# Optimization experiments

Hardware: AMD Instinct MI355X
Metric: run time of the kernel (lower is better)

Reference implementation:

```python
import jax, jax.numpy as jnp
import numpy as np

CHEB_K = 3
DIM_IN = 2
HIDDEN = 64
EMBED_DIM = 10
NODE_NUM = 2048
BATCH = 32


def _gconv(x, supports, W, b, cheb_k=CHEB_K):
    # Chebyshev graph conv applied directly to x (equivalent to building
    # T_k(A) matrices then applying: T_k(A) x = 2 A T_{k-1}(A) x - T_{k-2}(A) x).
    xs = [x, jnp.einsum('nm,bmc->bnc', supports, x)]
    for _ in range(2, cheb_k):
        xs.append(2.0 * jnp.einsum('nm,bmc->bnc', supports, xs[-1]) - xs[-2])
    x_g = jnp.concatenate(xs, axis=-1)          # [B, N, cheb_k*C]
    return jnp.einsum('bni,io->bno', x_g, W) + b


def setup_inputs() -> dict:
    key = jax.random.key(0)
    ks = jax.random.split(key, 7)
    c_in = DIM_IN + HIDDEN                       # 66
    # xavier_normal-ish scale for weights
    def xavier(k, fan_in, fan_out):
        std = float(np.sqrt(2.0 / (fan_in + fan_out)))
        return jax.random.normal(k, (fan_in, fan_out), dtype=jnp.float32) * std
    return {
        'x': jax.random.normal(ks[0], (BATCH, NODE_NUM, DIM_IN), dtype=jnp.float32),
        'state': jax.random.normal(ks[1], (BATCH, NODE_NUM, HIDDEN), dtype=jnp.float32),
        'node_embeddings': jax.random.normal(ks[2], (NODE_NUM, EMBED_DIM), dtype=jnp.float32),
        'W_gate': xavier(ks[3], CHEB_K * c_in, 2 * HIDDEN),
        'b_gate': jnp.zeros((2 * HIDDEN,), dtype=jnp.float32),
        'W_update': xavier(ks[4], CHEB_K * c_in, HIDDEN),
        'b_update': jnp.zeros((HIDDEN,), dtype=jnp.float32),
    }


def reference(x, state, node_embeddings, W_gate, b_gate, W_update, b_update):
    # adaptive adjacency: softmax(relu(E E^T), axis=1)
    logits = jnp.einsum('nc,mc->nm', node_embeddings, node_embeddings)
    supports = jax.nn.softmax(jax.nn.relu(logits), axis=1)   # [N, N]

    input_and_state = jnp.concatenate([x, state], axis=-1)   # [B, N, dim_in+hidden]
    z_r = jax.nn.sigmoid(_gconv(input_and_state, supports, W_gate, b_gate))
    z, r = jnp.split(z_r, 2, axis=-1)                        # each [B, N, hidden]
    candidate = jnp.concatenate([x, z * state], axis=-1)
    hc = jnp.tanh(_gconv(candidate, supports, W_update, b_update))
    h = r * state + (1.0 - r) * hc
    return h
```

## Files before the change

kernel.cpp:

```cpp
#include <hip/hip_runtime.h>


typedef __bf16 bf16x8 __attribute__((ext_vector_type(8)));
typedef __bf16 bf16x4 __attribute__((ext_vector_type(4)));
typedef float  f32x4  __attribute__((ext_vector_type(4)));

#define GLB(p) ((__attribute__((address_space(1))) void*)(void*)(p))
#define LDS(p) ((__attribute__((address_space(3))) void*)(p))

__global__ void prologue_kernel(const float* __restrict__ E, __bf16* __restrict__ S,
                                const float* __restrict__ Wg, __bf16* __restrict__ WTg,
                                const float* __restrict__ Wu, __bf16* __restrict__ WTu) {
    const int bid = blockIdx.x;
    const int t = threadIdx.x;
    __shared__ float sm[4], ss[4];
    if (bid >= 2048) {
        const float* W = (bid < 2176) ? Wg : Wu;
        __bf16* WT = (bid < 2176) ? WTg : WTu;
        const int Nout = (bid < 2176) ? 128 : 64;
        const int id = (bid - ((bid < 2176) ? 2048 : 2176)) * 256 + t;
        const int o = id >> 8, k = id & 255;
        const int jj = (k >= 144) ? 2 : (k >= 72 ? 1 : 0);
        const int cc = k - 72 * jj;
        const bool ok = (o < Nout) && (cc < 66) && (k < 216);
        WT[id] = ok ? (__bf16)W[(size_t)(66 * jj + cc) * Nout + o] : (__bf16)0.f;
        return;
    }
    const int n = bid;
    const int l = t & 63, w = t >> 6;
    float en[10];
#pragma unroll
    for (int i = 0; i < 10; ++i) en[i] = E[n * 10 + i];
    float vals[8];
    float mx = 0.f;
#pragma unroll
    for (int q = 0; q < 8; ++q) {
        const int m = q * 256 + t;
        const float* em = E + (size_t)m * 10;
        float d = 0.f;
#pragma unroll
        for (int i = 0; i < 10; ++i) d += en[i] * em[i];
        d = fmaxf(d, 0.f);
        vals[q] = d;
        mx = fmaxf(mx, d);
    }
#pragma unroll
    for (int off = 32; off; off >>= 1) mx = fmaxf(mx, __shfl_xor(mx, off));
    if (l == 0) sm[w] = mx;
    __syncthreads();
    mx = fmaxf(fmaxf(sm[0], sm[1]), fmaxf(sm[2], sm[3]));
    float sum = 0.f;
#pragma unroll
    for (int q = 0; q < 8; ++q) { vals[q] = __expf(vals[q] - mx); sum += vals[q]; }
#pragma unroll
    for (int off = 32; off; off >>= 1) sum += __shfl_xor(sum, off);
    if (l == 0) ss[w] = sum;
    __syncthreads();
    sum = ss[0] + ss[1] + ss[2] + ss[3];
    const float inv = 1.f / sum;
#pragma unroll
    for (int q = 0; q < 8; ++q) S[(size_t)n * 2048 + q * 256 + t] = (__bf16)(vals[q] * inv);
}

__global__ __launch_bounds__(256, 2)
void build_t2(const float* __restrict__ x, const float* __restrict__ st,
              const __bf16* __restrict__ zr, __bf16* __restrict__ T,
              __bf16* __restrict__ G) {
    __shared__ float Ls[66 * 129];
    const int b  = blockIdx.x >> 4;
    const int n0 = (blockIdx.x & 15) << 7;
    const int t = threadIdx.x;
    const size_t mb = (size_t)b * 2048 + n0;
    if (t < 128) {
        const float2 v = *(const float2*)&x[(mb + t) * 2];
        Ls[t] = v.x;
        Ls[129 + t] = v.y;
    }
#pragma unroll
    for (int r = 0; r < 8; ++r) {
        const int task = r * 256 + t;
        const int q = task & 15, n = task >> 4;
        f32x4 v = *(const f32x4*)&st[(mb + n) * 64 + q * 4];
        if (zr) {
            const bf16x4 z = *(const bf16x4*)&zr[(mb + n) * 128 + q * 4];
#pragma unroll
            for (int j = 0; j < 4; ++j) v[j] *= (float)z[j];
        }
        const int base = (2 + q * 4) * 129 + n;
#pragma unroll
        for (int j = 0; j < 4; ++j) Ls[base + j * 129] = v[j];
    }
    __syncthreads();
#pragma unroll
    for (int r = 0; r < 5; ++r) {
        const int task = r * 256 + t;
        if (task < 1056) {
            const int c = task >> 4, seg = task & 15;
            const float* src = &Ls[c * 129 + seg * 8];
            bf16x8 o;
#pragma unroll
            for (int j = 0; j < 8; ++j) o[j] = (__bf16)src[j];
            *(bf16x8*)&T[(size_t)(b * 66 + c) * 2048 + n0 + seg * 8] = o;
        }
    }
    {
        const int n = t & 127, half = t >> 7;
        const size_t grow = ((size_t)(b * 2048 + n0 + n)) * 256;
        for (int oct = half * 5; oct < (half ? 9 : 5); ++oct) {
            bf16x8 o8;
#pragma unroll
            for (int j = 0; j < 8; ++j) {
                const int cc = oct * 8 + j;
                o8[j] = (cc < 66) ? (__bf16)Ls[cc * 129 + n] : (__bf16)0.f;
            }
            *(bf16x8*)&G[grow + oct * 8] = o8;
        }
    }
}

__global__ __launch_bounds__(256, 3)
void gemm_pipe(const __bf16* __restrict__ A, int lda,
               const __bf16* __restrict__ Bt, int ldb,
               int K, int epi, int swz,
               __bf16* __restrict__ outT, const __bf16* __restrict__ subT,
               float* __restrict__ outF, const float* __restrict__ bias,
               __bf16* __restrict__ zrO, const __bf16* __restrict__ zrI,
               const float* __restrict__ state,
               __bf16* __restrict__ Gout, int gsec) {
    __shared__ __align__(16) __bf16 As[2][128 * 64];
    __shared__ __align__(16) __bf16 Bs[2][64 * 64];
    int mt, ct;
    if (swz) { mt = blockIdx.x & 15; ct = blockIdx.x >> 4; }
    else     { mt = blockIdx.x;      ct = blockIdx.y; }
    const int m0 = mt * 128, c0 = ct * 64;
    const int t = threadIdx.x;
    const int l = t & 63, w = t >> 6;
    const int wr = w >> 1, wc = w & 1;
    const int lm = l & 15, kq = l >> 4, lm7 = lm & 7;
    const int sr = l >> 3;
    const int gsw = (l & 7) ^ sr;

    f32x4 acc[4][2];
#pragma unroll
    for (int i = 0; i < 4; ++i)
#pragma unroll
        for (int j = 0; j < 2; ++j) acc[i][j] = (f32x4)0.f;

    const __bf16* Asrc = A  + (size_t)(m0 + w * 8 + sr) * lda + gsw * 8;
    const __bf16* Bsrc = Bt + (size_t)(c0 + w * 8 + sr) * ldb + gsw * 8;
    const int dstA = w * 512 + l * 8;

    auto stage = [&](int buf, int k0) {
#pragma unroll
        for (int q = 0; q < 4; ++q)
            __builtin_amdgcn_global_load_lds(GLB(Asrc + (size_t)q * 32 * lda + k0),
                                             LDS(&As[buf][q * 2048 + dstA]), 16, 0, 0);
#pragma unroll
        for (int q = 0; q < 2; ++q)
            __builtin_amdgcn_global_load_lds(GLB(Bsrc + (size_t)q * 32 * ldb + k0),
                                             LDS(&Bs[buf][q * 2048 + dstA]), 16, 0, 0);
    };
    auto compute = [&](int buf) {
        const __bf16* Ab = &As[buf][0];
        const __bf16* Bb = &Bs[buf][0];
#pragma unroll
        for (int ks = 0; ks < 2; ++ks) {
            const int ga = (((ks << 2) | kq) ^ lm7) << 3;
            bf16x8 af[4], bfr[2];
#pragma unroll
            for (int i = 0; i < 4; ++i)
                af[i] = *(const bf16x8*)&Ab[(wr * 64 + i * 16 + lm) * 64 + ga];
#pragma unroll
            for (int j = 0; j < 2; ++j)
                bfr[j] = *(const bf16x8*)&Bb[(wc * 32 + j * 16 + lm) * 64 + ga];
#pragma unroll
            for (int i = 0; i < 4; ++i)
#pragma unroll
                for (int j = 0; j < 2; ++j)
                    acc[i][j] = __builtin_amdgcn_mfma_f32_16x16x32_bf16(af[i], bfr[j], acc[i][j], 0, 0, 0);
        }
    };

    stage(0, 0);
    const int iters = K >> 6;
    for (int i = 0; i + 2 <= iters; i += 2) {
        stage(1, (i + 1) << 6);
        __builtin_amdgcn_sched_barrier(0);
        __builtin_amdgcn_s_waitcnt(0x0F76);
        __builtin_amdgcn_s_barrier();
        __builtin_amdgcn_sched_barrier(0);
        compute(0);
        __builtin_amdgcn_sched_barrier(0);
        __builtin_amdgcn_s_barrier();
        __builtin_amdgcn_sched_barrier(0);
        if (i + 2 < iters) {
            stage(0, (i + 2) << 6);
            __builtin_amdgcn_sched_barrier(0);
            __builtin_amdgcn_s_waitcnt(0x0F76);
        } else {
            __builtin_amdgcn_s_waitcnt(0x0F70);
        }
        __builtin_amdgcn_s_barrier();
        __builtin_amdgcn_sched_barrier(0);
        compute(1);
        __builtin_amdgcn_sched_barrier(0);
        if (i + 4 <= iters) {
            __builtin_amdgcn_s_barrier();
            __builtin_amdgcn_sched_barrier(0);
        }
    }

    const int rb0 = m0 + wr * 64 + kq * 4;
    const int cb0 = c0 + wc * 32 + lm;
#pragma unroll
    for (int i = 0; i < 4; ++i) {
        const int rbase = rb0 + i * 16;
#pragma unroll
        for (int j = 0; j < 2; ++j) {
            const int c = cb0 + j * 16;
            f32x4 v = acc[i][j];
            if (epi <= 1) {
                bf16x4 pk;
                if (epi == 0) {
#pragma unroll
                    for (int r = 0; r < 4; ++r) pk[r] = (__bf16)v[r];
                    *(bf16x4*)&outT[(size_t)c * 2048 + rbase] = pk;
                } else {
                    bf16x4 s = *(const bf16x4*)&subT[(size_t)c * 2048 + rbase];
#pragma unroll
                    for (int r = 0; r < 4; ++r) pk[r] = (__bf16)(2.f * v[r] - (float)s[r]);
                }
                const int b = c / 66, cc = c - b * 66;
                const size_t gb = ((size_t)(b * 2048 + rbase)) * 256 + gsec + cc;
#pragma unroll
                for (int r = 0; r < 4; ++r) Gout[gb + (size_t)r * 256] = pk[r];
            } else if (epi == 2) {
                const float bb = bias[c];
#pragma unroll
                for (int r = 0; r < 4; ++r) {
                    float xx = fminf(fmaxf(v[r] + bb, -30.f), 30.f);
                    zrO[(size_t)(rbase + r) * 128 + c] = (__bf16)(1.f / (1.f + __expf(-xx)));
                }
            } else {
                if (c < 64) {
                    const float bb = bias[c];
#pragma unroll
                    for (int r = 0; r < 4; ++r) {
                        const int m = rbase + r;
                        float xx = fminf(fmaxf(v[r] + bb, -15.f), 15.f);
                        float e = __expf(2.f * xx);
                        float hc = (e - 1.f) / (e + 1.f);
                        float rr = (float)zrI[(size_t)m * 128 + 64 + c];
                        float s = state[(size_t)m * 64 + c];
                        outF[(size_t)m * 64 + c] = rr * s + (1.f - rr) * hc;
                    }
                }
            }
        }
    }
}

extern "C" void kernel_launch(void* const* d_in, const int* in_sizes, int n_in,
                              void* d_out, int out_size, void* d_ws, size_t ws_size,
                              hipStream_t stream) {
    (void)in_sizes; (void)n_in; (void)out_size; (void)ws_size;
    const float* x  = (const float*)d_in[0];
    const float* st = (const float*)d_in[1];
    const float* E  = (const float*)d_in[2];
    const float* Wg = (const float*)d_in[3];
    const float* bg = (const float*)d_in[4];
    const float* Wu = (const float*)d_in[5];
    const float* bu = (const float*)d_in[6];
    float* out = (float*)d_out;

    char* p = (char*)d_ws;
    __bf16* S   = (__bf16*)p; p += (size_t)2048 * 2048 * 2;
    __bf16* T0  = (__bf16*)p; p += (size_t)2112 * 2048 * 2;
    __bf16* T1  = (__bf16*)p; p += (size_t)2112 * 2048 * 2;
    __bf16* G   = (__bf16*)p; p += (size_t)65536 * 256 * 2;
    __bf16* ZR  = (__bf16*)p; p += (size_t)65536 * 128 * 2;
    __bf16* WTg = (__bf16*)p; p += 128 * 256 * 2;
    __bf16* WTu = (__bf16*)p; p += 128 * 256 * 2;

    prologue_kernel<<<2304, 256, 0, stream>>>(E, S, Wg, WTg, Wu, WTu);

    build_t2<<<512, 256, 0, stream>>>(x, st, nullptr, T0, G);
    gemm_pipe<<<528, 256, 0, stream>>>(S, 2048, T0, 2048, 2048, 0, 1, T1, nullptr, nullptr, nullptr, nullptr, nullptr, nullptr, G, 72);
    gemm_pipe<<<528, 256, 0, stream>>>(S, 2048, T1, 2048, 2048, 1, 1, nullptr, T0, nullptr, nullptr, nullptr, nullptr, nullptr, G, 144);
    gemm_pipe<<<dim3(512, 2), 256, 0, stream>>>(G, 256, WTg, 256, 256, 2, 0, nullptr, nullptr, nullptr, bg, ZR, nullptr, nullptr, nullptr, 0);

    build_t2<<<512, 256, 0, stream>>>(x, st, ZR, T0, G);
    gemm_pipe<<<528, 256, 0, stream>>>(S, 2048, T0, 2048, 2048, 0, 1, T1, nullptr, nullptr, nullptr, nullptr, nullptr, nullptr, G, 72);
    gemm_pipe<<<528, 256, 0, stream>>>(S, 2048, T1, 2048, 2048, 1, 1, nullptr, T0, nullptr, nullptr, nullptr, nullptr, nullptr, G, 144);
    gemm_pipe<<<dim3(512, 1), 256, 0, stream>>>(G, 256, WTu, 256, 256, 3, 0, nullptr, nullptr, out, bu, nullptr, ZR, st, nullptr, 0);
}
```

Baseline: 265.5 us.

## Add dedicated weight-projection GEMM with whole-W LDS residency and swizzled layout

Replaces the generic pipelined GEMM used for the two small K=256 weight projections with a specialized kernel. The new kernel loads the entire transposed weight matrix into LDS once via direct global-to-LDS loads, reads A fragments straight from global memory, and covers all output columns in one block. The prologue now writes the weights in an XOR-swizzled layout to avoid LDS bank conflicts. This removes the double-buffered pipeline overhead and the duplicate A reads from the second column tile, at the cost of larger LDS use (up to 64KB) and lower occupancy.

```diff
diff --git a/kernel.cpp b/kernel.cpp
--- a/kernel.cpp
+++ b/kernel.cpp
@@ -23,7 +23,10 @@
         const int jj = (k >= 144) ? 2 : (k >= 72 ? 1 : 0);
         const int cc = k - 72 * jj;
         const bool ok = (o < Nout) && (cc < 66) && (k < 216);
-        WT[id] = ok ? (__bf16)W[(size_t)(66 * jj + cc) * Nout + o] : (__bf16)0.f;
+        const int q = k >> 3;
+        const int slot = (q & 24) | ((q & 7) ^ (o & 7));
+        WT[o * 256 + slot * 8 + (k & 7)] =
+            ok ? (__bf16)W[(size_t)(66 * jj + cc) * Nout + o] : (__bf16)0.f;
         return;
     }
     const int n = bid;
@@ -123,9 +126,6 @@
                const __bf16* __restrict__ Bt, int ldb,
                int K, int epi, int swz,
                __bf16* __restrict__ outT, const __bf16* __restrict__ subT,
-               float* __restrict__ outF, const float* __restrict__ bias,
-               __bf16* __restrict__ zrO, const __bf16* __restrict__ zrI,
-               const float* __restrict__ state,
                __bf16* __restrict__ Gout, int gsec) {
     __shared__ __align__(16) __bf16 As[2][128 * 64];
     __shared__ __align__(16) __bf16 Bs[2][64 * 64];
@@ -219,41 +219,98 @@
         for (int j = 0; j < 2; ++j) {
             const int c = cb0 + j * 16;
             f32x4 v = acc[i][j];
-            if (epi <= 1) {
-                bf16x4 pk;
-                if (epi == 0) {
-#pragma unroll
-                    for (int r = 0; r < 4; ++r) pk[r] = (__bf16)v[r];
-                    *(bf16x4*)&outT[(size_t)c * 2048 + rbase] = pk;
-                } else {
-                    bf16x4 s = *(const bf16x4*)&subT[(size_t)c * 2048 + rbase];
-#pragma unroll
-                    for (int r = 0; r < 4; ++r) pk[r] = (__bf16)(2.f * v[r] - (float)s[r]);
-                }
-                const int b = c / 66, cc = c - b * 66;
-                const size_t gb = ((size_t)(b * 2048 + rbase)) * 256 + gsec + cc;
-#pragma unroll
-                for (int r = 0; r < 4; ++r) Gout[gb + (size_t)r * 256] = pk[r];
-            } else if (epi == 2) {
-                const float bb = bias[c];
+            bf16x4 pk;
+            if (epi == 0) {
+#pragma unroll
+                for (int r = 0; r < 4; ++r) pk[r] = (__bf16)v[r];
+                *(bf16x4*)&outT[(size_t)c * 2048 + rbase] = pk;
+            } else {
+                bf16x4 s = *(const bf16x4*)&subT[(size_t)c * 2048 + rbase];
+#pragma unroll
+                for (int r = 0; r < 4; ++r) pk[r] = (__bf16)(2.f * v[r] - (float)s[r]);
+            }
+            const int b = c / 66, cc = c - b * 66;
+            const size_t gb = ((size_t)(b * 2048 + rbase)) * 256 + gsec + cc;
+#pragma unroll
+            for (int r = 0; r < 4; ++r) Gout[gb + (size_t)r * 256] = pk[r];
+        }
+    }
+}
+
+template <int NC>
+__global__ __launch_bounds__(256, 2)
+void gemm_w(const __bf16* __restrict__ G, const __bf16* __restrict__ WT,
+            const float* __restrict__ bias, int epi,
+            __bf16* __restrict__ zrO, const __bf16* __restrict__ zrI,
+            const float* __restrict__ state, float* __restrict__ outF) {
+    __shared__ __align__(16) __bf16 Ls[NC * 32 * 256];
+    const int t = threadIdx.x;
+    const int l = t & 63, w = t >> 6;
+    const int wr = w >> 1, wc = w & 1;
+    const int lm = l & 15, kq = l >> 4;
+    const int m0 = blockIdx.x * 128;
+
+#pragma unroll
+    for (int it = 0; it < NC * 4; ++it)
+        __builtin_amdgcn_global_load_lds(GLB(WT + it * 2048 + t * 8),
+                                         LDS(&Ls[it * 2048 + t * 8]), 16, 0, 0);
+    __builtin_amdgcn_s_waitcnt(0x0F70);
+    __syncthreads();
+
+    f32x4 acc[4][NC];
+#pragma unroll
+    for (int i = 0; i < 4; ++i)
+#pragma unroll
+        for (int j = 0; j < NC; ++j) acc[i][j] = (f32x4)0.f;
+
+    const __bf16* Arow = G + (size_t)(m0 + wr * 64 + lm) * 256 + kq * 8;
+    const int cw = wc * NC * 16;
+
+#pragma unroll
+    for (int ks = 0; ks < 8; ++ks) {
+        bf16x8 af[4], bfr[NC];
+#pragma unroll
+        for (int i = 0; i < 4; ++i)
+            af[i] = *(const bf16x8*)&Arow[(size_t)i * 16 * 256 + ks * 32];
+#pragma unroll
+        for (int j = 0; j < NC; ++j) {
+            const int o = cw + j * 16 + lm;
+            const int q = ks * 4 + kq;
+            const int slot = (q & 24) | ((q & 7) ^ (o & 7));
+            bfr[j] = *(const bf16x8*)&Ls[o * 256 + slot * 8];
+        }
+#pragma unroll
+        for (int i = 0; i < 4; ++i)
+#pragma unroll
+            for (int j = 0; j < NC; ++j)
+                acc[i][j] = __builtin_amdgcn_mfma_f32_16x16x32_bf16(af[i], bfr[j], acc[i][j], 0, 0, 0);
+    }
+
+    const int rb0 = m0 + wr * 64 + kq * 4;
+#pragma unroll
+    for (int i = 0; i < 4; ++i) {
+        const int rbase = rb0 + i * 16;
+#pragma unroll
+        for (int j = 0; j < NC; ++j) {
+            const int c = cw + j * 16 + lm;
+            const float bb = bias[c];
+            f32x4 v = acc[i][j];
+            if (epi == 2) {
 #pragma unroll
                 for (int r = 0; r < 4; ++r) {
                     float xx = fminf(fmaxf(v[r] + bb, -30.f), 30.f);
                     zrO[(size_t)(rbase + r) * 128 + c] = (__bf16)(1.f / (1.f + __expf(-xx)));
                 }
             } else {
-                if (c < 64) {
-                    const float bb = bias[c];
-#pragma unroll
-                    for (int r = 0; r < 4; ++r) {
-                        const int m = rbase + r;
-                        float xx = fminf(fmaxf(v[r] + bb, -15.f), 15.f);
-                        float e = __expf(2.f * xx);
-                        float hc = (e - 1.f) / (e + 1.f);
-                        float rr = (float)zrI[(size_t)m * 128 + 64 + c];
-                        float s = state[(size_t)m * 64 + c];
-                        outF[(size_t)m * 64 + c] = rr * s + (1.f - rr) * hc;
-                    }
+#pragma unroll
+                for (int r = 0; r < 4; ++r) {
+                    const int m = rbase + r;
+                    float xx = fminf(fmaxf(v[r] + bb, -15.f), 15.f);
+                    float e = __expf(2.f * xx);
+                    float hc = (e - 1.f) / (e + 1.f);
+                    float rr = (float)zrI[(size_t)m * 128 + 64 + c];
+                    float s = state[(size_t)m * 64 + c];
+                    outF[(size_t)m * 64 + c] = rr * s + (1.f - rr) * hc;
                 }
             }
         }
@@ -285,12 +342,12 @@
     prologue_kernel<<<2304, 256, 0, stream>>>(E, S, Wg, WTg, Wu, WTu);
 
     build_t2<<<512, 256, 0, stream>>>(x, st, nullptr, T0, G);
-    gemm_pipe<<<528, 256, 0, stream>>>(S, 2048, T0, 2048, 2048, 0, 1, T1, nullptr, nullptr, nullptr, nullptr, nullptr, nullptr, G, 72);
-    gemm_pipe<<<528, 256, 0, stream>>>(S, 2048, T1, 2048, 2048, 1, 1, nullptr, T0, nullptr, nullptr, nullptr, nullptr, nullptr, G, 144);
-    gemm_pipe<<<dim3(512, 2), 256, 0, stream>>>(G, 256, WTg, 256, 256, 2, 0, nullptr, nullptr, nullptr, bg, ZR, nullptr, nullptr, nullptr, 0);
+    gemm_pipe<<<528, 256, 0, stream>>>(S, 2048, T0, 2048, 2048, 0, 1, T1, nullptr, G, 72);
+    gemm_pipe<<<528, 256, 0, stream>>>(S, 2048, T1, 2048, 2048, 1, 1, nullptr, T0, G, 144);
+    gemm_w<4><<<512, 256, 0, stream>>>(G, WTg, bg, 2, ZR, nullptr, nullptr, nullptr);
 
     build_t2<<<512, 256, 0, stream>>>(x, st, ZR, T0, G);
-    gemm_pipe<<<528, 256, 0, stream>>>(S, 2048, T0, 2048, 2048, 0, 1, T1, nullptr, nullptr, nullptr, nullptr, nullptr, nullptr, G, 72);
-    gemm_pipe<<<528, 256, 0, stream>>>(S, 2048, T1, 2048, 2048, 1, 1, nullptr, T0, nullptr, nullptr, nullptr, nullptr, nullptr, G, 144);
-    gemm_pipe<<<dim3(512, 1), 256, 0, stream>>>(G, 256, WTu, 256, 256, 3, 0, nullptr, nullptr, out, bu, nullptr, ZR, st, nullptr, 0);
-}
+    gemm_pipe<<<528, 256, 0, stream>>>(S, 2048, T0, 2048, 2048, 0, 1, T1, nullptr, G, 72);
+    gemm_pipe<<<528, 256, 0, stream>>>(S, 2048, T1, 2048, 2048, 1, 1, nullptr, T0, G, 144);
+    gemm_w<2><<<512, 256, 0, stream>>>(G, WTu, bu, 3, nullptr, ZR, st, out);
+}
```

New measurement: 268.3 us. No clear change (+1.1%).
